# Optimization experiments

Measured on AMD Instinct MI355X. Metric: run time of the kernel, lower is better.

The kernel has to match this reference:

```python
import jax, jax.numpy as jnp
import numpy as np
import math

N, E, D, H, L = 50000, 800000, 256, 8, 8
DK = D // H
DFF = 4 * D


def _layernorm(h, g, b, eps=1e-5):
    m = jnp.mean(h, axis=-1, keepdims=True)
    v = jnp.mean((h - m) ** 2, axis=-1, keepdims=True)
    return (h - m) * jax.lax.rsqrt(v + eps) * g + b


def setup_inputs() -> dict:
    key = jax.random.key(0)
    ks = jax.random.split(key, 16)
    s = 1.0 / math.sqrt(D)
    x = jax.random.normal(ks[0], (N, D), dtype=jnp.float32)
    # every node gets >=1 in-edge so z > 0 everywhere (as in real connected graphs)
    edge_src = jax.random.randint(ks[1], (E,), 0, N, dtype=jnp.int32)
    edge_dst = jnp.concatenate([
        jnp.arange(N, dtype=jnp.int32),
        jax.random.randint(ks[2], (E - N,), 0, N, dtype=jnp.int32),
    ])
    return {
        "x": x,
        "edge_src": edge_src,
        "edge_dst": edge_dst,
        "Wq": jax.random.normal(ks[3], (L, D, D), dtype=jnp.float32) * s,
        "bq": jnp.zeros((L, D), dtype=jnp.float32),
        "Wk": jax.random.normal(ks[4], (L, D, D), dtype=jnp.float32) * s,
        "Wv": jax.random.normal(ks[5], (L, D, D), dtype=jnp.float32) * s,
        "Wo": jax.random.normal(ks[6], (L, D, D), dtype=jnp.float32) * s,
        "bo": jnp.zeros((L, D), dtype=jnp.float32),
        "ln1_g": jnp.ones((L, D), dtype=jnp.float32),
        "ln1_b": jnp.zeros((L, D), dtype=jnp.float32),
        "W1": jax.random.normal(ks[7], (L, D, DFF), dtype=jnp.float32) * s,
        "b1": jnp.zeros((L, DFF), dtype=jnp.float32),
        "W2": jax.random.normal(ks[8], (L, DFF, D), dtype=jnp.float32) * (1.0 / math.sqrt(DFF)),
        "b2": jnp.zeros((L, D), dtype=jnp.float32),
        "ln2_g": jnp.ones((L, D), dtype=jnp.float32),
        "ln2_b": jnp.zeros((L, D), dtype=jnp.float32),
    }


def _layer(x, src, dst, Wq, bq, Wk, Wv, Wo, bo, g1, b1n, W1, b1, W2, b2, g2, b2n):
    n = x.shape[0]
    q = (x @ Wq + bq).reshape(n, H, DK)
    k = (x @ Wk).reshape(n, H, DK)
    v = (x @ Wv).reshape(n, H, DK)
    # edge score: src_dot_dst('k','q') -> [E, H]
    score = jnp.einsum('ehd,ehd->eh', k[src], q[dst])
    # scaled_exp: exp(clamp(score / sqrt(d_k), -5, 5))
    score = jnp.exp(jnp.clip(score / math.sqrt(DK), -5.0, 5.0))
    # u_mul_e + sum aggregation -> wv [N, H, DK]; copy_edge + sum -> z [N, H]
    msg = v[src] * score[:, :, None]
    wv = jax.ops.segment_sum(msg, dst, num_segments=n)
    z = jax.ops.segment_sum(score, dst, num_segments=n)
    o = (wv / z[:, :, None]).reshape(n, D)
    h = _layernorm(x + o @ Wo + bo, g1, b1n)
    # FFN with residual + layernorm
    ff = jax.nn.relu(h @ W1 + b1) @ W2 + b2
    return _layernorm(h + ff, g2, b2n)


def reference(x, edge_src, edge_dst, Wq, bq, Wk, Wv, Wo, bo, ln1_g, ln1_b,
              W1, b1, W2, b2, ln2_g, ln2_b):
    for i in range(L):
        x = _layer(x, edge_src, edge_dst, Wq[i], bq[i], Wk[i], Wv[i], Wo[i],
                   bo[i], ln1_g[i], ln1_b[i], W1[i], b1[i], W2[i], b2[i],
                   ln2_g[i], ln2_b[i])
    return x
```

## Files before the change

### kernel.cpp

```cpp
#include <hip/hip_runtime.h>
#include <cstdint>
#include <cstddef>

#define D 256
#define H 8
#define DFF 1024

typedef short s16x8 __attribute__((ext_vector_type(8)));
typedef float f32x4 __attribute__((ext_vector_type(4)));

static inline int cdiv(int a, int b) { return (a + b - 1) / b; }

__device__ inline uint16_t f2bf(float x) {
    unsigned u = __float_as_uint(x);
    u += 0x7FFFu + ((u >> 16) & 1u);
    return (uint16_t)(u >> 16);
}
__device__ inline float bf2f(uint16_t h) {
    return __uint_as_float(((unsigned)h) << 16);
}

__device__ inline void gload_lds16(const void* g, void* l) {
    __builtin_amdgcn_global_load_lds(
        (const __attribute__((address_space(1))) void*)g,
        (__attribute__((address_space(3))) void*)l, 16, 0, 0);
}

__device__ inline void vmcnt0() { asm volatile("s_waitcnt vmcnt(0)" ::: "memory"); }
__device__ inline void vmcnt4() { asm volatile("s_waitcnt vmcnt(4)" ::: "memory"); }
__device__ inline void vmcnt5() { asm volatile("s_waitcnt vmcnt(5)" ::: "memory"); }
__device__ inline void lgkm0()  { asm volatile("s_waitcnt lgkmcnt(0)" ::: "memory"); }
#define SB0() __builtin_amdgcn_sched_barrier(0)
#define BARF() do { SB0(); __builtin_amdgcn_s_barrier(); SB0(); } while (0)

__global__ __launch_bounds__(256) void zero_int_kernel(int* __restrict__ p, int count)
{
    int i = blockIdx.x * blockDim.x + threadIdx.x;
    if (i < count) p[i] = 0;
}

__global__ __launch_bounds__(256) void count_deg_kernel(
    const int* __restrict__ edst, int* __restrict__ deg, int E)
{
    int e = blockIdx.x * blockDim.x + threadIdx.x;
    if (e < E) atomicAdd(&deg[edst[e]], 1);
}

__global__ __launch_bounds__(256) void block_sum_kernel(
    const int* __restrict__ deg, int* __restrict__ bsum, int N)
{
    int t = threadIdx.x;
    int gid = blockIdx.x * 256 + t;
    int val = (gid < N) ? deg[gid] : 0;
    #pragma unroll
    for (int o = 1; o < 64; o <<= 1) val += __shfl_xor(val, o);
    __shared__ int r[4];
    if ((t & 63) == 0) r[t >> 6] = val;
    __syncthreads();
    if (t == 0) bsum[blockIdx.x] = r[0] + r[1] + r[2] + r[3];
}

__global__ __launch_bounds__(256) void scan_bsum_kernel(int* __restrict__ bsum, int nb)
{
    __shared__ int tmp[256];
    int t = threadIdx.x;
    int val = (t < nb) ? bsum[t] : 0;
    tmp[t] = val;
    __syncthreads();
    for (int off = 1; off < 256; off <<= 1) {
        int add = (t >= off) ? tmp[t - off] : 0;
        __syncthreads();
        tmp[t] += add;
        __syncthreads();
    }
    if (t < nb) bsum[t] = tmp[t] - val;
}

__global__ __launch_bounds__(256) void scan_write_kernel(
    const int* __restrict__ deg, const int* __restrict__ bsum,
    int* __restrict__ rowptr, int* __restrict__ cursor, int N)
{
    __shared__ int tmp[256];
    int t = threadIdx.x;
    int gid = blockIdx.x * 256 + t;
    int val = (gid < N) ? deg[gid] : 0;
    tmp[t] = val;
    __syncthreads();
    for (int off = 1; off < 256; off <<= 1) {
        int add = (t >= off) ? tmp[t - off] : 0;
        __syncthreads();
        tmp[t] += add;
        __syncthreads();
    }
    int excl = tmp[t] - val + bsum[blockIdx.x];
    if (gid < N) { rowptr[gid] = excl; cursor[gid] = excl; }
    if (gid == N - 1) rowptr[N] = excl + val;
}

__global__ __launch_bounds__(256) void fill_csr_kernel(
    const int* __restrict__ esrc, const int* __restrict__ edst,
    int* __restrict__ cursor, int* __restrict__ csr_src, int E)
{
    int e = blockIdx.x * blockDim.x + threadIdx.x;
    if (e < E) {
        int pos = atomicAdd(&cursor[edst[e]], 1);
        csr_src[pos] = esrc[e];
    }
}

__global__ __launch_bounds__(256) void transpose_cast_kernel(
    const float* __restrict__ in, uint16_t* __restrict__ out,
    int R, int C, size_t inLS, size_t outLS)
{
    __shared__ float t[32][33];
    in  += blockIdx.z * inLS;
    out += blockIdx.z * outLS;
    int c0 = blockIdx.x * 32, r0 = blockIdx.y * 32;
    int tx = threadIdx.x, ty = threadIdx.y;
    #pragma unroll
    for (int i = 0; i < 4; ++i)
        t[ty + i * 8][tx] = in[(size_t)(r0 + ty + i * 8) * C + c0 + tx];
    __syncthreads();
    #pragma unroll
    for (int i = 0; i < 4; ++i)
        out[(size_t)(c0 + ty + i * 8) * R + r0 + tx] = f2bf(t[tx][ty + i * 8]);
}

__global__ __launch_bounds__(256) void cast_f32_bf16_kernel(
    const float* __restrict__ in, uint16_t* __restrict__ out, int n4)
{
    int i = blockIdx.x * blockDim.x + threadIdx.x;
    if (i >= n4) return;
    float4 f = ((const float4*)in)[i];
    uint16_t o0 = f2bf(f.x), o1 = f2bf(f.y), o2 = f2bf(f.z), o3 = f2bf(f.w);
    uint2 pk;
    pk.x = (unsigned)o0 | ((unsigned)o1 << 16);
    pk.y = (unsigned)o2 | ((unsigned)o3 << 16);
    ((uint2*)out)[i] = pk;
}

__global__ __launch_bounds__(256) void build_qkv_bias_kernel(
    const float* __restrict__ bq, float* __restrict__ qb, int total)
{
    int i = blockIdx.x * blockDim.x + threadIdx.x;
    if (i >= total) return;
    int l = i / 768, c = i - l * 768;
    qb[i] = (c < 256) ? bq[l * 256 + c] : 0.f;
}

__global__ __launch_bounds__(256) void gemm_bf16_kernel(
    const uint16_t* __restrict__ A, int lda, int M, int K,
    const uint16_t* __restrict__ BT, int Nc,
    const float* __restrict__ bias,
    uint16_t* __restrict__ Cb, int relu)
{
    __shared__ __align__(16) uint16_t As[2][128 * 32];
    __shared__ __align__(16) uint16_t Bs[2][128 * 32];

    const int tid  = threadIdx.x;
    const int lane = tid & 63;
    const int w    = tid >> 6;
    const int wr   = w >> 1, wc = w & 1;
    const int quad = lane >> 4;
    const int l15  = lane & 15;

    const int nwg = gridDim.x * gridDim.y;
    const int lin = blockIdx.y * gridDim.x + blockIdx.x;
    const int xcd = lin & 7, idx = lin >> 3;
    const int q8 = nwg >> 3, r8 = nwg & 7;
    const int lin2 = (xcd < r8 ? xcd * (q8 + 1) : r8 * (q8 + 1) + (xcd - r8) * q8) + idx;
    const int mt = lin2 % gridDim.x;
    const int nt = lin2 / gridDim.x;

    const int m0 = mt * 128;
    const int n0 = nt * 128;

    f32x4 acc[4][4] = {};

    const int jbase = w * 2;
    const int srow  = lane >> 2;
    const int skc   = (lane & 3) * 8;

    auto stage = [&](int b, int k0) {
        #pragma unroll
        for (int jj = 0; jj < 2; ++jj) {
            int j = jbase + jj;
            int r = j * 16 + srow;
            int gr = m0 + r; if (gr > M - 1) gr = M - 1;
            gload_lds16(A  + (size_t)gr * lda + k0 + skc, &As[b][j * 512]);
            gload_lds16(BT + (size_t)(n0 + r) * K + k0 + skc, &Bs[b][j * 512]);
        }
    };

    const int nsteps = K >> 5;
    stage(0, 0);
    for (int s = 0; s < nsteps; ++s) {
        if (s + 1 < nsteps) { stage((s + 1) & 1, (s + 1) << 5); vmcnt4(); }
        else vmcnt0();
        BARF();
        const int b = s & 1;
        s16x8 af[4], bf[4];
        #pragma unroll
        for (int t = 0; t < 4; ++t) {
            af[t] = *(const s16x8*)&As[b][(wr * 64 + t * 16 + l15) * 32 + quad * 8];
            bf[t] = *(const s16x8*)&Bs[b][(wc * 64 + t * 16 + l15) * 32 + quad * 8];
        }
        #pragma unroll
        for (int i = 0; i < 4; ++i)
            #pragma unroll
            for (int jt = 0; jt < 4; ++jt)
                acc[i][jt] = __builtin_amdgcn_mfma_f32_16x16x32_bf16(
                    af[i], bf[jt], acc[i][jt], 0, 0, 0);
        BARF();
    }

    float bv[4];
    #pragma unroll
    for (int jt = 0; jt < 4; ++jt)
        bv[jt] = bias ? bias[n0 + wc * 64 + jt * 16 + l15] : 0.f;

    #pragma unroll
    for (int i = 0; i < 4; ++i) {
        #pragma unroll
        for (int r = 0; r < 4; ++r) {
            int m = m0 + wr * 64 + i * 16 + quad * 4 + r;
            if (m >= M) continue;
            #pragma unroll
            for (int jt = 0; jt < 4; ++jt) {
                int n = n0 + wc * 64 + jt * 16 + l15;
                float val = acc[i][jt][r] + bv[jt];
                if (relu) val = fmaxf(val, 0.f);
                Cb[(size_t)m * Nc + n] = f2bf(val);
            }
        }
    }
}

__global__ __launch_bounds__(256) void gemm_ln_kernel(
    const uint16_t* __restrict__ A, int lda, int M, int K,
    const uint16_t* __restrict__ BT,
    const float* __restrict__ bias,
    const float* __restrict__ resid,
    const float* __restrict__ g, const float* __restrict__ b,
    float* __restrict__ Cf, uint16_t* __restrict__ Cb)
{
    __shared__ __align__(16) uint16_t As[2][64 * 32];
    __shared__ __align__(16) uint16_t Bs[2][256 * 32];
    __shared__ float sS[64][4];
    __shared__ float sQ[64][4];

    const int tid  = threadIdx.x;
    const int lane = tid & 63;
    const int w    = tid >> 6;
    const int quad = lane >> 4;
    const int l15  = lane & 15;

    const int m0 = blockIdx.x * 64;

    f32x4 acc[4][4] = {};

    auto stage = [&](int bb, int k0) {
        {
            int r = tid >> 2, kc = (tid & 3) * 8;
            int gr = m0 + r; if (gr > M - 1) gr = M - 1;
            gload_lds16(A + (size_t)gr * lda + k0 + kc, &As[bb][tid * 8]);
        }
        #pragma unroll
        for (int i = 0; i < 4; ++i) {
            int slot = i * 256 + tid;
            int n = slot >> 2, kc = (slot & 3) * 8;
            gload_lds16(BT + (size_t)n * K + k0 + kc, &Bs[bb][slot * 8]);
        }
    };

    const int nsteps = K >> 5;
    stage(0, 0);
    for (int s = 0; s < nsteps; ++s) {
        if (s + 1 < nsteps) { stage((s + 1) & 1, (s + 1) << 5); vmcnt5(); }
        else vmcnt0();
        BARF();
        const int bb = s & 1;
        s16x8 af[4], bf[4];
        #pragma unroll
        for (int t = 0; t < 4; ++t) {
            af[t] = *(const s16x8*)&As[bb][(t * 16 + l15) * 32 + quad * 8];
            bf[t] = *(const s16x8*)&Bs[bb][(w * 64 + t * 16 + l15) * 32 + quad * 8];
        }
        #pragma unroll
        for (int i = 0; i < 4; ++i)
            #pragma unroll
            for (int jt = 0; jt < 4; ++jt)
                acc[i][jt] = __builtin_amdgcn_mfma_f32_16x16x32_bf16(
                    af[i], bf[jt], acc[i][jt], 0, 0, 0);
        BARF();
    }

    float bv[4], gv[4], bbv[4];
    #pragma unroll
    for (int jt = 0; jt < 4; ++jt) {
        int n = w * 64 + jt * 16 + l15;
        bv[jt]  = bias[n];
        gv[jt]  = g[n];
        bbv[jt] = b[n];
    }

    #pragma unroll
    for (int i = 0; i < 4; ++i) {
        #pragma unroll
        for (int r = 0; r < 4; ++r) {
            int ml = i * 16 + quad * 4 + r;
            int m  = m0 + ml;
            bool valid = (m < M);
            float s = 0.f, s2 = 0.f;
            #pragma unroll
            for (int jt = 0; jt < 4; ++jt) {
                int n = w * 64 + jt * 16 + l15;
                float val = acc[i][jt][r] + bv[jt];
                if (valid) val += resid[(size_t)m * 256 + n];
                acc[i][jt][r] = val;
                s += val;
                s2 += val * val;
            }
            #pragma unroll
            for (int o = 1; o < 16; o <<= 1) {
                s  += __shfl_xor(s, o);
                s2 += __shfl_xor(s2, o);
            }
            if (l15 == 0) { sS[ml][w] = s; sQ[ml][w] = s2; }
        }
    }
    __syncthreads();

    #pragma unroll
    for (int i = 0; i < 4; ++i) {
        #pragma unroll
        for (int r = 0; r < 4; ++r) {
            int ml = i * 16 + quad * 4 + r;
            int m  = m0 + ml;
            if (m >= M) continue;
            float s  = sS[ml][0] + sS[ml][1] + sS[ml][2] + sS[ml][3];
            float s2 = sQ[ml][0] + sQ[ml][1] + sQ[ml][2] + sQ[ml][3];
            float mean = s * (1.f / 256.f);
            float var  = s2 * (1.f / 256.f) - mean * mean;
            float rstd = rsqrtf(var + 1e-5f);
            #pragma unroll
            for (int jt = 0; jt < 4; ++jt) {
                int n = w * 64 + jt * 16 + l15;
                float out = (acc[i][jt][r] - mean) * rstd * gv[jt] + bbv[jt];
                Cf[(size_t)m * 256 + n] = out;
                if (Cb) Cb[(size_t)m * 256 + n] = f2bf(out);
            }
        }
    }
}

__global__ __launch_bounds__(256) void ffn_fused_kernel(
    const uint16_t* __restrict__ A,
    int M,
    const uint16_t* __restrict__ BT1,
    const float* __restrict__ b1,
    const uint16_t* __restrict__ BT2,
    const float* __restrict__ b2,
    const float* __restrict__ resid,
    const float* __restrict__ g, const float* __restrict__ b,
    float* __restrict__ Cf, uint16_t* __restrict__ Cb)
{
    __shared__ __align__(16) uint16_t U[2][8192];
    __shared__ __align__(16) uint16_t Ts[128][144];

    const int tid  = threadIdx.x;
    const int lane = tid & 63;
    const int w    = tid >> 6;
    const int quad = lane >> 4;
    const int l15  = lane & 15;
    const int m0   = blockIdx.x * 128;

    f32x4 acc2[8][4] = {};

    auto issue = [&](int q) {
        if (q >= 96) return;
        const int slot = q & 1;
        const int c = q / 12;
        const int r = q - c * 12;
        const int row = tid >> 2, kc = (tid & 3) * 8;
        if (r < 8) {
            const int k0 = r << 5;
            #pragma unroll
            for (int i = 0; i < 2; ++i) {
                int rr = row + i * 64;
                int gr = m0 + rr; if (gr > M - 1) gr = M - 1;
                gload_lds16(A + (size_t)gr * 256 + k0 + kc,
                            &U[slot][(i * 256 + tid) * 8]);
            }
            #pragma unroll
            for (int i = 0; i < 2; ++i) {
                int rr = row + i * 64;
                gload_lds16(BT1 + (size_t)(c * 128 + rr) * 256 + k0 + kc,
                            &U[slot][4096 + (i * 256 + tid) * 8]);
            }
        } else {
            const int ts = r - 8;
            #pragma unroll
            for (int i = 0; i < 4; ++i) {
                int rr = row + i * 64;
                gload_lds16(BT2 + (size_t)rr * 1024 + c * 128 + ts * 32 + kc,
                            &U[slot][(i * 256 + tid) * 8]);
            }
        }
    };

    issue(0);

    for (int c = 0; c < 8; ++c) {
        f32x4 acc1[8][2] = {};
        const int pb = c * 12;

        for (int ks = 0; ks < 8; ++ks) {
            const int p = pb + ks;
            issue(p + 1);
            vmcnt4();
            BARF();
            const uint16_t* Us = U[p & 1];
            s16x8 bf1[2];
            #pragma unroll
            for (int jt = 0; jt < 2; ++jt)
                bf1[jt] = *(const s16x8*)&Us[4096 + (w * 32 + jt * 16 + l15) * 32 + quad * 8];
            #pragma unroll
            for (int i = 0; i < 8; ++i) {
                s16x8 af = *(const s16x8*)&Us[(i * 16 + l15) * 32 + quad * 8];
                acc1[i][0] = __builtin_amdgcn_mfma_f32_16x16x32_bf16(
                    af, bf1[0], acc1[i][0], 0, 0, 0);
                acc1[i][1] = __builtin_amdgcn_mfma_f32_16x16x32_bf16(
                    af, bf1[1], acc1[i][1], 0, 0, 0);
            }
            BARF();
        }

        {
            float bv1[2];
            #pragma unroll
            for (int jt = 0; jt < 2; ++jt)
                bv1[jt] = b1[c * 128 + w * 32 + jt * 16 + l15];
            #pragma unroll
            for (int i = 0; i < 8; ++i)
                #pragma unroll
                for (int r = 0; r < 4; ++r) {
                    int ml = i * 16 + quad * 4 + r;
                    #pragma unroll
                    for (int jt = 0; jt < 2; ++jt) {
                        float val = acc1[i][jt][r] + bv1[jt];
                        val = fmaxf(val, 0.f);
                        Ts[ml][w * 32 + jt * 16 + l15] = f2bf(val);
                    }
                }
        }
        lgkm0();
        BARF();

        for (int ts = 0; ts < 4; ++ts) {
            const int p = pb + 8 + ts;
            issue(p + 1);
            if (p == 95) vmcnt0(); else vmcnt4();
            BARF();
            const uint16_t* Us = U[p & 1];
            s16x8 bf2[4];
            #pragma unroll
            for (int jt = 0; jt < 4; ++jt)
                bf2[jt] = *(const s16x8*)&Us[(w * 64 + jt * 16 + l15) * 32 + quad * 8];
            #pragma unroll
            for (int i = 0; i < 8; ++i) {
                s16x8 af2 = *(const s16x8*)&Ts[i * 16 + l15][ts * 32 + quad * 8];
                #pragma unroll
                for (int jt = 0; jt < 4; ++jt)
                    acc2[i][jt] = __builtin_amdgcn_mfma_f32_16x16x32_bf16(
                        af2, bf2[jt], acc2[i][jt], 0, 0, 0);
            }
            BARF();
        }
    }

    float* sS = (float*)&U[0][0];
    float* sQ = (float*)&U[0][1024];

    float bv[4], gv[4], bbv[4];
    #pragma unroll
    for (int jt = 0; jt < 4; ++jt) {
        int n = w * 64 + jt * 16 + l15;
        bv[jt]  = b2[n];
        gv[jt]  = g[n];
        bbv[jt] = b[n];
    }

    #pragma unroll
    for (int i = 0; i < 8; ++i) {
        #pragma unroll
        for (int r = 0; r < 4; ++r) {
            int ml = i * 16 + quad * 4 + r;
            int m  = m0 + ml;
            bool valid = (m < M);
            float s = 0.f, s2 = 0.f;
            #pragma unroll
            for (int jt = 0; jt < 4; ++jt) {
                float val = acc2[i][jt][r] + bv[jt];
                if (valid) val += resid[(size_t)m * 256 + w * 64 + jt * 16 + l15];
                acc2[i][jt][r] = val;
                s += val;
                s2 += val * val;
            }
            #pragma unroll
            for (int o = 1; o < 16; o <<= 1) {
                s  += __shfl_xor(s, o);
                s2 += __shfl_xor(s2, o);
            }
            if (l15 == 0) { sS[ml * 4 + w] = s; sQ[ml * 4 + w] = s2; }
        }
    }
    __syncthreads();

    #pragma unroll
    for (int i = 0; i < 8; ++i) {
        #pragma unroll
        for (int r = 0; r < 4; ++r) {
            int ml = i * 16 + quad * 4 + r;
            int m  = m0 + ml;
            if (m >= M) continue;
            float s  = sS[ml * 4 + 0] + sS[ml * 4 + 1] + sS[ml * 4 + 2] + sS[ml * 4 + 3];
            float s2 = sQ[ml * 4 + 0] + sQ[ml * 4 + 1] + sQ[ml * 4 + 2] + sQ[ml * 4 + 3];
            float mean = s * (1.f / 256.f);
            float var  = s2 * (1.f / 256.f) - mean * mean;
            float rstd = rsqrtf(var + 1e-5f);
            #pragma unroll
            for (int jt = 0; jt < 4; ++jt) {
                int n = w * 64 + jt * 16 + l15;
                float out = (acc2[i][jt][r] - mean) * rstd * gv[jt] + bbv[jt];
                Cf[(size_t)m * 256 + n] = out;
                if (Cb) Cb[(size_t)m * 256 + n] = f2bf(out);
            }
        }
    }
}

__global__ __launch_bounds__(256) void node_attn_kernel(
    uint16_t* __restrict__ qkv,
    const int* __restrict__ rowptr, const int* __restrict__ csr_src, int N)
{
    int node = (blockIdx.x * blockDim.x + threadIdx.x) >> 6;
    int lane = threadIdx.x & 63;
    if (node >= N) return;

    uint16_t* qp = qkv + (size_t)node * 768 + lane * 4;
    uint2 qu = *(const uint2*)qp;
    float q0 = bf2f((uint16_t)(qu.x & 0xFFFF)), q1 = bf2f((uint16_t)(qu.x >> 16));
    float q2 = bf2f((uint16_t)(qu.y & 0xFFFF)), q3 = bf2f((uint16_t)(qu.y >> 16));

    float a0 = 0.f, a1 = 0.f, a2 = 0.f, a3 = 0.f, zacc = 0.f;
    const float inv_sqrt_dk = 0.17677669529663687f;

    int beg = rowptr[node], end = rowptr[node + 1];
    int i = beg;
    for (; i + 1 < end; i += 2) {
        int s0 = csr_src[i], s1 = csr_src[i + 1];
        const uint16_t* b0 = qkv + (size_t)s0 * 768;
        const uint16_t* b1 = qkv + (size_t)s1 * 768;
        uint2 ku0 = *(const uint2*)(b0 + 256 + lane * 4);
        uint2 ku1 = *(const uint2*)(b1 + 256 + lane * 4);
        uint2 vu0 = *(const uint2*)(b0 + 512 + lane * 4);
        uint2 vu1 = *(const uint2*)(b1 + 512 + lane * 4);

        float p0 = bf2f((uint16_t)(ku0.x & 0xFFFF)) * q0
                 + bf2f((uint16_t)(ku0.x >> 16))   * q1
                 + bf2f((uint16_t)(ku0.y & 0xFFFF)) * q2
                 + bf2f((uint16_t)(ku0.y >> 16))   * q3;
        float p1 = bf2f((uint16_t)(ku1.x & 0xFFFF)) * q0
                 + bf2f((uint16_t)(ku1.x >> 16))   * q1
                 + bf2f((uint16_t)(ku1.y & 0xFFFF)) * q2
                 + bf2f((uint16_t)(ku1.y >> 16))   * q3;
        p0 += __shfl_xor(p0, 1); p1 += __shfl_xor(p1, 1);
        p0 += __shfl_xor(p0, 2); p1 += __shfl_xor(p1, 2);
        p0 += __shfl_xor(p0, 4); p1 += __shfl_xor(p1, 4);
        float sc0 = __expf(fminf(fmaxf(p0 * inv_sqrt_dk, -5.f), 5.f));
        float sc1 = __expf(fminf(fmaxf(p1 * inv_sqrt_dk, -5.f), 5.f));

        a0 += bf2f((uint16_t)(vu0.x & 0xFFFF)) * sc0;
        a1 += bf2f((uint16_t)(vu0.x >> 16))   * sc0;
        a2 += bf2f((uint16_t)(vu0.y & 0xFFFF)) * sc0;
        a3 += bf2f((uint16_t)(vu0.y >> 16))   * sc0;
        zacc += sc0;
        a0 += bf2f((uint16_t)(vu1.x & 0xFFFF)) * sc1;
        a1 += bf2f((uint16_t)(vu1.x >> 16))   * sc1;
        a2 += bf2f((uint16_t)(vu1.y & 0xFFFF)) * sc1;
        a3 += bf2f((uint16_t)(vu1.y >> 16))   * sc1;
        zacc += sc1;
    }
    if (i < end) {
        int s = csr_src[i];
        const uint16_t* base = qkv + (size_t)s * 768;
        uint2 ku = *(const uint2*)(base + 256 + lane * 4);
        float p = bf2f((uint16_t)(ku.x & 0xFFFF)) * q0
                + bf2f((uint16_t)(ku.x >> 16))   * q1
                + bf2f((uint16_t)(ku.y & 0xFFFF)) * q2
                + bf2f((uint16_t)(ku.y >> 16))   * q3;
        p += __shfl_xor(p, 1);
        p += __shfl_xor(p, 2);
        p += __shfl_xor(p, 4);
        float sc = __expf(fminf(fmaxf(p * inv_sqrt_dk, -5.f), 5.f));
        uint2 vu = *(const uint2*)(base + 512 + lane * 4);
        a0 += bf2f((uint16_t)(vu.x & 0xFFFF)) * sc;
        a1 += bf2f((uint16_t)(vu.x >> 16))   * sc;
        a2 += bf2f((uint16_t)(vu.y & 0xFFFF)) * sc;
        a3 += bf2f((uint16_t)(vu.y >> 16))   * sc;
        zacc += sc;
    }
    float inv = 1.f / zacc;
    uint2 pk;
    pk.x = (unsigned)f2bf(a0 * inv) | ((unsigned)f2bf(a1 * inv) << 16);
    pk.y = (unsigned)f2bf(a2 * inv) | ((unsigned)f2bf(a3 * inv) << 16);
    *(uint2*)qp = pk;
}

extern "C" void kernel_launch(void* const* d_in, const int* in_sizes, int n_in,
                              void* d_out, int out_size, void* d_ws, size_t ws_size,
                              hipStream_t stream)
{
    const float* x0   = (const float*)d_in[0];
    const int* esrc   = (const int*)d_in[1];
    const int* edst   = (const int*)d_in[2];
    const float* Wq   = (const float*)d_in[3];
    const float* bq   = (const float*)d_in[4];
    const float* Wk   = (const float*)d_in[5];
    const float* Wv   = (const float*)d_in[6];
    const float* Wo   = (const float*)d_in[7];
    const float* bo   = (const float*)d_in[8];
    const float* ln1g = (const float*)d_in[9];
    const float* ln1b = (const float*)d_in[10];
    const float* W1   = (const float*)d_in[11];
    const float* b1   = (const float*)d_in[12];
    const float* W2   = (const float*)d_in[13];
    const float* b2   = (const float*)d_in[14];
    const float* ln2g = (const float*)d_in[15];
    const float* ln2b = (const float*)d_in[16];

    const int N = in_sizes[0] / D;
    const int E = in_sizes[1];
    const int L = in_sizes[3] / (D * D);
    const size_t ND = (size_t)N * D;

    char* p = (char*)d_ws;
    float* bufX = (float*)p;         p += ND * 4;
    uint16_t* xb  = (uint16_t*)p;    p += ND * 2;
    uint16_t* qkv = (uint16_t*)p;    p += (size_t)N * 768 * 2;
    uint16_t* hb  = (uint16_t*)p;    p += ND * 2;
    uint16_t* BTqkv = (uint16_t*)p;  p += (size_t)L * 768 * 256 * 2;
    uint16_t* BTo   = (uint16_t*)p;  p += (size_t)L * 256 * 256 * 2;
    uint16_t* BT1   = (uint16_t*)p;  p += (size_t)L * 1024 * 256 * 2;
    uint16_t* BT2   = (uint16_t*)p;  p += (size_t)L * 256 * 1024 * 2;
    float* qbias    = (float*)p;     p += (size_t)L * 768 * 4;
    int* rowptr  = (int*)p;          p += (size_t)(N + 1) * 4;
    int* cursor  = (int*)p;          p += (size_t)N * 4;
    int* deg     = cursor;
    int* csr_src = (int*)p;          p += (size_t)E * 4;
    int* bsum    = (int*)p;

    const int nb = cdiv(N, 256);
    dim3 blk(256);
    int edgeBlocks = cdiv(E, 256);
    int nodeBlocks = cdiv(N, 4);

    dim3 tb(32, 8);
    transpose_cast_kernel<<<dim3(8, 8, L), tb, 0, stream>>>(Wq, BTqkv, 256, 256, (size_t)65536, (size_t)768 * 256);
    transpose_cast_kernel<<<dim3(8, 8, L), tb, 0, stream>>>(Wk, BTqkv + 256 * 256, 256, 256, (size_t)65536, (size_t)768 * 256);
    transpose_cast_kernel<<<dim3(8, 8, L), tb, 0, stream>>>(Wv, BTqkv + 512 * 256, 256, 256, (size_t)65536, (size_t)768 * 256);
    transpose_cast_kernel<<<dim3(8, 8, L), tb, 0, stream>>>(Wo, BTo, 256, 256, (size_t)65536, (size_t)65536);
    transpose_cast_kernel<<<dim3(32, 8, L), tb, 0, stream>>>(W1, BT1, 256, 1024, (size_t)262144, (size_t)262144);
    transpose_cast_kernel<<<dim3(8, 32, L), tb, 0, stream>>>(W2, BT2, 1024, 256, (size_t)262144, (size_t)262144);
    build_qkv_bias_kernel<<<cdiv(L * 768, 256), blk, 0, stream>>>(bq, qbias, L * 768);
    cast_f32_bf16_kernel<<<cdiv((int)(ND / 4), 256), blk, 0, stream>>>(x0, xb, (int)(ND / 4));

    zero_int_kernel<<<cdiv(N, 256), blk, 0, stream>>>(deg, N);
    count_deg_kernel<<<edgeBlocks, blk, 0, stream>>>(edst, deg, E);
    block_sum_kernel<<<nb, blk, 0, stream>>>(deg, bsum, N);
    scan_bsum_kernel<<<1, blk, 0, stream>>>(bsum, nb);
    scan_write_kernel<<<nb, blk, 0, stream>>>(deg, bsum, rowptr, cursor, N);
    fill_csr_kernel<<<edgeBlocks, blk, 0, stream>>>(esrc, edst, cursor, csr_src, E);

    const int Mt128 = cdiv(N, 128);
    const int Mt64  = cdiv(N, 64);
    dim3 gQKV(Mt128, 768 / 128);
    dim3 gLN(Mt64, 1);
    dim3 gFFN(Mt128, 1);

    for (int l = 0; l < L; ++l) {
        const uint16_t* BTqkv_l = BTqkv + (size_t)l * 768 * 256;
        const uint16_t* BTo_l   = BTo + (size_t)l * 65536;
        const uint16_t* BT1_l   = BT1 + (size_t)l * 262144;
        const uint16_t* BT2_l   = BT2 + (size_t)l * 262144;
        const float* xin_f = (l == 0) ? x0 : bufX;

        gemm_bf16_kernel<<<gQKV, blk, 0, stream>>>(xb, 256, N, 256, BTqkv_l, 768,
            qbias + (size_t)l * 768, qkv, 0);

        node_attn_kernel<<<nodeBlocks, blk, 0, stream>>>(qkv, rowptr, csr_src, N);

        gemm_ln_kernel<<<gLN, blk, 0, stream>>>(qkv, 768, N, 256, BTo_l,
            bo + (size_t)l * 256, xin_f, ln1g + (size_t)l * 256, ln1b + (size_t)l * 256,
            bufX, hb);

        float* fout = (l == L - 1) ? (float*)d_out : bufX;
        ffn_fused_kernel<<<gFFN, blk, 0, stream>>>(hb, N, BT1_l,
            b1 + (size_t)l * 1024, BT2_l, b2 + (size_t)l * 256, bufX,
            ln2g + (size_t)l * 256, ln2b + (size_t)l * 256,
            fout, (l == L - 1) ? nullptr : xb);

        xin_f = bufX;
    }
}
```

Baseline: 3.519 ms.

## Restructure fused FFN: 64-row tiles, resident A, per-wave weight buffers, swizzled LDS

The fused FFN kernel now processes 64 rows per block instead of 128 and loads the whole 64x256 activation tile into LDS once. Each wave streams only its own slice of W1/W2 into a private double buffer, which removes the block-wide barriers from the inner k-loops. LDS layouts for A, the hidden tile and the weight slices use XOR swizzles to avoid bank conflicts. In exchange, twice as many blocks each re-stream the full weight matrices, so weight traffic from L2 doubles, and the per-wave waitcnt logic is more fragile.

```diff
diff --git a/kernel.cpp b/kernel.cpp
--- a/kernel.cpp
+++ b/kernel.cpp
@@ -27,11 +27,14 @@
 }
 
 __device__ inline void vmcnt0() { asm volatile("s_waitcnt vmcnt(0)" ::: "memory"); }
+__device__ inline void vmcnt2() { asm volatile("s_waitcnt vmcnt(2)" ::: "memory"); }
 __device__ inline void vmcnt4() { asm volatile("s_waitcnt vmcnt(4)" ::: "memory"); }
 __device__ inline void vmcnt5() { asm volatile("s_waitcnt vmcnt(5)" ::: "memory"); }
 __device__ inline void lgkm0()  { asm volatile("s_waitcnt lgkmcnt(0)" ::: "memory"); }
 #define SB0() __builtin_amdgcn_sched_barrier(0)
 #define BARF() do { SB0(); __builtin_amdgcn_s_barrier(); SB0(); } while (0)
+
+#define MFMA(a, b, c) __builtin_amdgcn_mfma_f32_16x16x32_bf16((a), (b), (c), 0, 0, 0)
 
 __global__ __launch_bounds__(256) void zero_int_kernel(int* __restrict__ p, int count)
 {
@@ -209,8 +212,7 @@
         for (int i = 0; i < 4; ++i)
             #pragma unroll
             for (int jt = 0; jt < 4; ++jt)
-                acc[i][jt] = __builtin_amdgcn_mfma_f32_16x16x32_bf16(
-                    af[i], bf[jt], acc[i][jt], 0, 0, 0);
+                acc[i][jt] = MFMA(af[i], bf[jt], acc[i][jt]);
         BARF();
     }
 
@@ -290,8 +292,7 @@
         for (int i = 0; i < 4; ++i)
             #pragma unroll
             for (int jt = 0; jt < 4; ++jt)
-                acc[i][jt] = __builtin_amdgcn_mfma_f32_16x16x32_bf16(
-                    af[i], bf[jt], acc[i][jt], 0, 0, 0);
+                acc[i][jt] = MFMA(af[i], bf[jt], acc[i][jt]);
         BARF();
     }
 
@@ -365,122 +366,142 @@
     const float* __restrict__ g, const float* __restrict__ b,
     float* __restrict__ Cf, uint16_t* __restrict__ Cb)
 {
-    __shared__ __align__(16) uint16_t U[2][8192];
-    __shared__ __align__(16) uint16_t Ts[128][144];
+    __shared__ __align__(16) uint16_t Ares[64 * 256];
+    __shared__ __align__(16) uint16_t Ts[64 * 128];
+    __shared__ __align__(16) uint16_t WB[4][2][2048];
 
     const int tid  = threadIdx.x;
     const int lane = tid & 63;
     const int w    = tid >> 6;
     const int quad = lane >> 4;
     const int l15  = lane & 15;
-    const int m0   = blockIdx.x * 128;
-
-    f32x4 acc2[8][4] = {};
+    const int m0   = blockIdx.x * 64;
+
+    #pragma unroll
+    for (int i = 0; i < 8; ++i) {
+        int slot = i * 256 + tid;
+        int r = slot >> 5, gg = slot & 31;
+        int gr = m0 + r; if (gr > M - 1) gr = M - 1;
+        gload_lds16(A + (size_t)gr * 256 + ((gg ^ (r & 7)) * 8), &Ares[slot * 8]);
+    }
 
     auto issue = [&](int q) {
         if (q >= 96) return;
         const int slot = q & 1;
         const int c = q / 12;
         const int r = q - c * 12;
-        const int row = tid >> 2, kc = (tid & 3) * 8;
+        uint16_t* dst = &WB[w][slot][0];
         if (r < 8) {
             const int k0 = r << 5;
             #pragma unroll
             for (int i = 0; i < 2; ++i) {
-                int rr = row + i * 64;
-                int gr = m0 + rr; if (gr > M - 1) gr = M - 1;
-                gload_lds16(A + (size_t)gr * 256 + k0 + kc,
-                            &U[slot][(i * 256 + tid) * 8]);
-            }
-            #pragma unroll
-            for (int i = 0; i < 2; ++i) {
-                int rr = row + i * 64;
-                gload_lds16(BT1 + (size_t)(c * 128 + rr) * 256 + k0 + kc,
-                            &U[slot][4096 + (i * 256 + tid) * 8]);
+                int s2 = i * 64 + lane;
+                int rl = s2 >> 2, gg = s2 & 3;
+                gload_lds16(BT1 + (size_t)(c * 128 + w * 32 + rl) * 256 + k0
+                                + ((gg ^ ((rl >> 1) & 3)) * 8),
+                            dst + s2 * 8);
             }
         } else {
             const int ts = r - 8;
             #pragma unroll
             for (int i = 0; i < 4; ++i) {
-                int rr = row + i * 64;
-                gload_lds16(BT2 + (size_t)rr * 1024 + c * 128 + ts * 32 + kc,
-                            &U[slot][(i * 256 + tid) * 8]);
+                int s2 = i * 64 + lane;
+                int rl = s2 >> 2, gg = s2 & 3;
+                gload_lds16(BT2 + (size_t)(w * 64 + rl) * 1024 + c * 128 + ts * 32
+                                + ((gg ^ ((rl >> 1) & 3)) * 8),
+                            dst + s2 * 8);
             }
         }
     };
 
     issue(0);
+    vmcnt2();
+    BARF();
+
+    f32x4 acc2[4][4] = {};
 
     for (int c = 0; c < 8; ++c) {
-        f32x4 acc1[8][2] = {};
+        f32x4 acc1[4][2] = {};
         const int pb = c * 12;
 
+        #pragma unroll
         for (int ks = 0; ks < 8; ++ks) {
             const int p = pb + ks;
+            lgkm0(); SB0();
             issue(p + 1);
-            vmcnt4();
-            BARF();
-            const uint16_t* Us = U[p & 1];
+            if (ks < 7) vmcnt2(); else vmcnt4();
+            SB0();
+            const uint16_t* B1s = &WB[w][p & 1][0];
             s16x8 bf1[2];
             #pragma unroll
-            for (int jt = 0; jt < 2; ++jt)
-                bf1[jt] = *(const s16x8*)&Us[4096 + (w * 32 + jt * 16 + l15) * 32 + quad * 8];
-            #pragma unroll
-            for (int i = 0; i < 8; ++i) {
-                s16x8 af = *(const s16x8*)&Us[(i * 16 + l15) * 32 + quad * 8];
-                acc1[i][0] = __builtin_amdgcn_mfma_f32_16x16x32_bf16(
-                    af, bf1[0], acc1[i][0], 0, 0, 0);
-                acc1[i][1] = __builtin_amdgcn_mfma_f32_16x16x32_bf16(
-                    af, bf1[1], acc1[i][1], 0, 0, 0);
-            }
-            BARF();
-        }
-
+            for (int jt = 0; jt < 2; ++jt) {
+                int rl = jt * 16 + l15;
+                bf1[jt] = *(const s16x8*)&B1s[rl * 32 + ((quad ^ ((rl >> 1) & 3)) * 8)];
+            }
+            #pragma unroll
+            for (int i = 0; i < 4; ++i) {
+                int rr = i * 16 + l15;
+                s16x8 af = *(const s16x8*)&Ares[rr * 256
+                              + (((ks * 4 + quad) ^ (rr & 7)) * 8)];
+                acc1[i][0] = MFMA(af, bf1[0], acc1[i][0]);
+                acc1[i][1] = MFMA(af, bf1[1], acc1[i][1]);
+            }
+        }
+
+        BARF();
         {
             float bv1[2];
             #pragma unroll
             for (int jt = 0; jt < 2; ++jt)
                 bv1[jt] = b1[c * 128 + w * 32 + jt * 16 + l15];
             #pragma unroll
-            for (int i = 0; i < 8; ++i)
+            for (int i = 0; i < 4; ++i)
                 #pragma unroll
                 for (int r = 0; r < 4; ++r) {
                     int ml = i * 16 + quad * 4 + r;
                     #pragma unroll
                     for (int jt = 0; jt < 2; ++jt) {
+                        int col = w * 32 + jt * 16 + l15;
                         float val = acc1[i][jt][r] + bv1[jt];
                         val = fmaxf(val, 0.f);
-                        Ts[ml][w * 32 + jt * 16 + l15] = f2bf(val);
+                        Ts[ml * 128 + (((col >> 3) ^ (ml & 7)) * 8) + (col & 7)]
+                            = f2bf(val);
                     }
                 }
         }
         lgkm0();
         BARF();
 
+        #pragma unroll
         for (int ts = 0; ts < 4; ++ts) {
             const int p = pb + 8 + ts;
+            lgkm0(); SB0();
             issue(p + 1);
-            if (p == 95) vmcnt0(); else vmcnt4();
-            BARF();
-            const uint16_t* Us = U[p & 1];
+            if (ts < 3) vmcnt4();
+            else if (c < 7) vmcnt2();
+            else vmcnt0();
+            SB0();
+            const uint16_t* B2s = &WB[w][p & 1][0];
             s16x8 bf2[4];
             #pragma unroll
-            for (int jt = 0; jt < 4; ++jt)
-                bf2[jt] = *(const s16x8*)&Us[(w * 64 + jt * 16 + l15) * 32 + quad * 8];
-            #pragma unroll
-            for (int i = 0; i < 8; ++i) {
-                s16x8 af2 = *(const s16x8*)&Ts[i * 16 + l15][ts * 32 + quad * 8];
+            for (int jt = 0; jt < 4; ++jt) {
+                int rl = jt * 16 + l15;
+                bf2[jt] = *(const s16x8*)&B2s[rl * 32 + ((quad ^ ((rl >> 1) & 3)) * 8)];
+            }
+            #pragma unroll
+            for (int i = 0; i < 4; ++i) {
+                int rr = i * 16 + l15;
+                s16x8 af2 = *(const s16x8*)&Ts[rr * 128
+                               + (((ts * 4 + quad) ^ (rr & 7)) * 8)];
                 #pragma unroll
                 for (int jt = 0; jt < 4; ++jt)
-                    acc2[i][jt] = __builtin_amdgcn_mfma_f32_16x16x32_bf16(
-                        af2, bf2[jt], acc2[i][jt], 0, 0, 0);
-            }
-            BARF();
-        }
-    }
-
-    float* sS = (float*)&U[0][0];
-    float* sQ = (float*)&U[0][1024];
+                    acc2[i][jt] = MFMA(af2, bf2[jt], acc2[i][jt]);
+            }
+        }
+    }
+
+    float* sS = (float*)&Ares[0];
+    float* sQ = (float*)&Ares[512];
 
     float bv[4], gv[4], bbv[4];
     #pragma unroll
@@ -492,7 +513,7 @@
     }
 
     #pragma unroll
-    for (int i = 0; i < 8; ++i) {
+    for (int i = 0; i < 4; ++i) {
         #pragma unroll
         for (int r = 0; r < 4; ++r) {
             int ml = i * 16 + quad * 4 + r;
@@ -518,7 +539,7 @@
     __syncthreads();
 
     #pragma unroll
-    for (int i = 0; i < 8; ++i) {
+    for (int i = 0; i < 4; ++i) {
         #pragma unroll
         for (int r = 0; r < 4; ++r) {
             int ml = i * 16 + quad * 4 + r;
@@ -687,7 +708,6 @@
     const int Mt64  = cdiv(N, 64);
     dim3 gQKV(Mt128, 768 / 128);
     dim3 gLN(Mt64, 1);
-    dim3 gFFN(Mt128, 1);
 
     for (int l = 0; l < L; ++l) {
         const uint16_t* BTqkv_l = BTqkv + (size_t)l * 768 * 256;
@@ -706,7 +726,7 @@
             bufX, hb);
 
         float* fout = (l == L - 1) ? (float*)d_out : bufX;
-        ffn_fused_kernel<<<gFFN, blk, 0, stream>>>(hb, N, BT1_l,
+        ffn_fused_kernel<<<gLN, blk, 0, stream>>>(hb, N, BT1_l,
             b1 + (size_t)l * 1024, BT2_l, b2 + (size_t)l * 256, bufX,
             ln2g + (size_t)l * 256, ln2b + (size_t)l * 256,
             fout, (l == L - 1) ? nullptr : xb);
```

After: 3.706 ms. +5.3%, slower.
